# Kernel tuning notes

Hardware: AMD Instinct MI355X
Metric: run time of the kernel (lower is better)

The kernel has to match this reference:

```python
import jax, jax.numpy as jnp
import numpy as np

D_MODEL = 512
STATE_DIM = 6
D_STATE = 16
D_CONV = 4
EXPAND = 2
D_INNER = EXPAND * D_MODEL            # 1024
DT_RANK = -(-D_MODEL // 16)           # ceil(d_model/16) = 32


def setup_inputs() -> dict:
    key = jax.random.key(0)
    ks = jax.random.split(key, 12)
    s = 0.02
    return {
        "features": jax.random.normal(ks[0], (32, 2048, D_MODEL), dtype=jnp.float32),
        # Mamba params (mamba_ssm defaults: in/out_proj bias=False, conv+dt_proj bias=True)
        "in_proj_w": jax.random.normal(ks[1], (2 * D_INNER, D_MODEL), dtype=jnp.float32) * s,
        "conv_w": jax.random.normal(ks[2], (D_INNER, D_CONV), dtype=jnp.float32) * s,
        "conv_b": jnp.zeros((D_INNER,), dtype=jnp.float32),
        "x_proj_w": jax.random.normal(ks[3], (DT_RANK + 2 * D_STATE, D_INNER), dtype=jnp.float32) * s,
        "dt_proj_w": jax.random.normal(ks[4], (D_INNER, DT_RANK), dtype=jnp.float32) * s,
        "dt_proj_b": jax.random.normal(ks[5], (D_INNER,), dtype=jnp.float32) * s,
        "A_log": jnp.log(jnp.broadcast_to(jnp.arange(1, D_STATE + 1, dtype=jnp.float32), (D_INNER, D_STATE))),
        "D": jnp.ones((D_INNER,), dtype=jnp.float32),
        "out_proj_w": jax.random.normal(ks[6], (D_MODEL, D_INNER), dtype=jnp.float32) * s,
        # trailing fc head: d_model -> state_dim**2
        "fc_w": jax.random.normal(ks[7], (STATE_DIM * STATE_DIM, D_MODEL), dtype=jnp.float32) * s,
        "fc_b": jnp.zeros((STATE_DIM * STATE_DIM,), dtype=jnp.float32),
    }


def reference(features, in_proj_w, conv_w, conv_b, x_proj_w, dt_proj_w, dt_proj_b,
              A_log, D, out_proj_w, fc_w, fc_b):
    # Original loops Mamba over timesteps with seq_len=1 slices -> each timestep is
    # independent. Flatten (batch, seq) into one token axis and vectorize.
    B_, T, dm = features.shape
    f = features.reshape(B_ * T, dm)                      # (N, d_model)

    xz = f @ in_proj_w.T                                  # (N, 2*d_inner)
    x, z = jnp.split(xz, 2, axis=-1)
    # causal depthwise conv on a length-1 sequence: only the last tap contributes
    x = jax.nn.silu(x * conv_w[:, -1] + conv_b)           # (N, d_inner)

    x_dbl = x @ x_proj_w.T                                # (N, dt_rank + 2*d_state)
    dt = x_dbl[:, :DT_RANK]
    Bm = x_dbl[:, DT_RANK:DT_RANK + D_STATE]              # (N, d_state)
    Cm = x_dbl[:, DT_RANK + D_STATE:]                     # (N, d_state)
    delta = jax.nn.softplus(dt @ dt_proj_w.T + dt_proj_b) # (N, d_inner)

    # single-step selective scan with h0 = 0:
    #   h = exp(delta*A)*0 + delta*B*x ;  y = sum_s C_s h_s + D*x
    # (A_log therefore never affects the output for seq_len=1 calls)
    bc = jnp.sum(Bm * Cm, axis=-1, keepdims=True)         # (N, 1)
    y = delta * x * bc + D * x                            # (N, d_inner)
    y = y * jax.nn.silu(z)

    out = y @ out_proj_w.T                                # (N, d_model)
    A_flat = out @ fc_w.T + fc_b                          # (N, state_dim**2)
    return A_flat.reshape(B_, T, STATE_DIM, STATE_DIM)
```

## Files before the change

### kernel.cpp

```cpp
#include <hip/hip_runtime.h>

typedef unsigned short u16;
typedef unsigned int u32;
typedef __attribute__((ext_vector_type(8))) short bf16x8;
typedef __attribute__((ext_vector_type(4))) float f32x4;

#define NTOK 65536
#define DM 512
#define DI 1024

__device__ __forceinline__ float bf2f(u16 u){ u32 x=((u32)u)<<16; float f; __builtin_memcpy(&f,&x,4); return f; }
__device__ __forceinline__ u16 f2bf(float f){ u32 u; __builtin_memcpy(&u,&f,4); u += 0x7fffu + ((u>>16)&1u); return (u16)(u>>16); }
__device__ __forceinline__ float siluf(float x){ return x/(1.f+__expf(-x)); }
__device__ __forceinline__ float softplus_fast(float x){
  float l = __logf(1.f + __expf(x));
  return (x > 20.f) ? x : l;
}

__device__ __forceinline__ void gload_lds16(const void* g, void* l){
  __builtin_amdgcn_global_load_lds((const __attribute__((address_space(1))) u32*)g,
                                   (__attribute__((address_space(3))) u32*)l, 16, 0, 0);
}

__global__ void k_sentinel(float* out){ out[0] = 1.2345e6f; }

__global__ void k_cast_bf16(const float* __restrict__ in, u16* __restrict__ out, int n){
  int i = (blockIdx.x*256 + threadIdx.x)*4;
  if (i >= n) return;
  float4 v = *(const float4*)(in + i);
  ushort4 o; o.x=f2bf(v.x); o.y=f2bf(v.y); o.z=f2bf(v.z); o.w=f2bf(v.w);
  *(ushort4*)(out + i) = o;
}

__global__ void k_make_wa(const float* __restrict__ fcw, const float* __restrict__ opw,
                          u16* __restrict__ wa){
  int j = blockIdx.x*256 + threadIdx.x;
  int i = blockIdx.y;
  float s = 0.f;
  if (i < 36){
    const float* fr = fcw + i*DM;
    #pragma unroll 8
    for (int k=0;k<DM;++k) s += fr[k]*opw[(size_t)k*DI + j];
  }
  wa[(size_t)i*DI + j] = f2bf(s);
}

__global__ __launch_bounds__(512) void k_gemm_xz(
  const u16* __restrict__ A, const u16* __restrict__ B,
  const float* __restrict__ convw, const float* __restrict__ convb,
  u16* __restrict__ xp, u16* __restrict__ zs)
{
  __shared__ u16 smem[49152];
  const int tid=threadIdx.x, wv=tid>>6, ln=tid&63;
  const int l15=ln&15, l4=ln>>4, h=l15&7;
  const int d = blockIdx.x;
  const int xcd = d & 7, q = d >> 3;
  const int g = xcd + 8*(q >> 4);
  const int mcb = q & 15;
  const int r0 = g*128, c0g = mcb*128;
  const int wm=wv>>1, wn=wv&1;
  const int sr=ln>>3, scs=((ln&7)^sr)*8;
  const int chk0=(l4^h)*8, chk1=((l4+4)^h)*8;
  f32x4 acc[2][4]={};

  auto STAGE=[&](int buf, int kt){
    const int k0 = kt*64;
    u16* Ad = smem + buf*16384;
    u16* Bd = Ad + 8192;
    #pragma unroll
    for (int it=0;it<2;++it){
      int c=wv*2+it;
      gload_lds16(A + (size_t)(r0 + c*8 + sr)*DM + k0 + scs, Ad + c*512);
    }
    #pragma unroll
    for (int it=0;it<2;++it){
      int c=wv*2+it;
      gload_lds16(B + (size_t)(c0g + c*8 + sr)*DM + k0 + scs, Bd + c*512);
    }
  };

  STAGE(0,0); STAGE(1,1);
  #pragma clang loop unroll(disable)
  for (int t=0;t<8;++t){
    if (t<7) asm volatile("s_waitcnt vmcnt(4)" ::: "memory");
    else     asm volatile("s_waitcnt vmcnt(0)" ::: "memory");
    __builtin_amdgcn_s_barrier();
    __builtin_amdgcn_sched_barrier(0);
    if (t+2<8) STAGE((t+2)%3, t+2);
    const u16* Ac = smem + (t%3)*16384;
    const u16* Bc = Ac + 8192;
    #pragma unroll
    for (int kk=0;kk<2;++kk){
      const int ch = kk ? chk1 : chk0;
      bf16x8 af[2], bfr[4];
      #pragma unroll
      for (int m=0;m<2;++m) af[m]=*(const bf16x8*)(Ac + (wm*32+m*16+l15)*64 + ch);
      #pragma unroll
      for (int n=0;n<4;++n) bfr[n]=*(const bf16x8*)(Bc + (wn*64+n*16+l15)*64 + ch);
      #pragma unroll
      for (int m=0;m<2;++m)
        #pragma unroll
        for (int n=0;n<4;++n)
          acc[m][n]=__builtin_amdgcn_mfma_f32_16x16x32_bf16(af[m],bfr[n],acc[m][n],0,0,0);
    }
    __builtin_amdgcn_sched_barrier(0);
  }
  __syncthreads();

  const bool isx = (c0g < DI);
  const int cc0 = isx ? c0g : c0g - DI;
  u16* ep = smem;
  #pragma unroll
  for (int n=0;n<4;++n){
    int tcol = wn*64 + n*16 + l15;
    int gcol = c0g + tcol;
    float cw = isx ? convw[gcol*4+3] : 0.f;
    float cb = isx ? convb[gcol]     : 0.f;
    #pragma unroll
    for (int m=0;m<2;++m){
      int trow = wm*32 + m*16 + l4*4;
      #pragma unroll
      for (int r=0;r<4;++r){
        float v = acc[m][n][r];
        float o = isx ? siluf(v*cw + cb) : siluf(v);
        ep[(trow+r)*160 + tcol] = f2bf(o);
      }
    }
  }
  __syncthreads();
  const int rrow = tid>>2, qq = tid&3;
  const u16* srcp = ep + rrow*160 + qq*32;
  u16* dst = (isx ? xp : zs) + (size_t)(r0+rrow)*DI + cc0 + qq*32;
  #pragma unroll
  for (int j=0;j<4;++j)
    ((int4*)dst)[j] = ((const int4*)srcp)[j];
}

template<int EPI>
__global__ __launch_bounds__(256) void k_gemm_n64(
  const u16* __restrict__ A, const u16* __restrict__ B,
  u16* __restrict__ dtb, float* __restrict__ bc,
  const float* __restrict__ fcb, float* __restrict__ out)
{
  __shared__ u16 smem[24576];
  u16* SA = smem;
  u16* SB = smem + 16384;
  const int tid=threadIdx.x, wv=tid>>6, ln=tid&63;
  const int l15=ln&15, l4=ln>>4, h=l15&7;
  const int r0=blockIdx.x*128;
  const int wm=wv>>1, wn=wv&1;
  const int sr=ln>>3, scs=((ln&7)^sr)*8;
  const int chk0=(l4^h)*8, chk1=((l4+4)^h)*8;
  const int rA=(wm*64+l15)*64, rB=(wn*32+l15)*64;
  f32x4 acc[4][2]={};

  auto STAGE=[&](int buf, int k0){
    u16* Ad = SA + buf*8192;
    u16* Bd = SB + buf*4096;
    #pragma unroll
    for (int it=0;it<4;++it){
      int c=wv*4+it;
      gload_lds16(A + (size_t)(r0 + c*8 + sr)*DI + k0 + scs, Ad + c*512);
    }
    #pragma unroll
    for (int it=0;it<2;++it){
      int c=wv*2+it;
      gload_lds16(B + (size_t)(c*8 + sr)*DI + k0 + scs, Bd + c*512);
    }
  };

  STAGE(0, 0);
  __syncthreads();
  __builtin_amdgcn_sched_barrier(0);
  int cur = 0;
  #pragma clang loop unroll(disable)
  for (int t=0;t<16;++t){
    if (t < 15) STAGE(cur^1, (t+1)*64);
    const u16* Ac = SA + cur*8192;
    const u16* Bc = SB + cur*4096;
    #pragma unroll
    for (int kk=0;kk<2;++kk){
      const int ch = kk ? chk1 : chk0;
      bf16x8 af[4], bfr[2];
      #pragma unroll
      for (int m=0;m<4;++m) af[m]=*(const bf16x8*)(Ac + rA + m*1024 + ch);
      #pragma unroll
      for (int n=0;n<2;++n) bfr[n]=*(const bf16x8*)(Bc + rB + n*1024 + ch);
      #pragma unroll
      for (int m=0;m<4;++m)
        #pragma unroll
        for (int n=0;n<2;++n)
          acc[m][n]=__builtin_amdgcn_mfma_f32_16x16x32_bf16(af[m],bfr[n],acc[m][n],0,0,0);
    }
    __syncthreads();
    __builtin_amdgcn_sched_barrier(0);
    cur ^= 1;
  }

  if (EPI==0){
    float* W = (float*)smem;
    #pragma unroll
    for (int n=0;n<2;++n){
      int j = wn*32 + n*16 + l15;
      #pragma unroll
      for (int m=0;m<4;++m){
        int trow = wm*64 + m*16 + l4*4;
        #pragma unroll
        for (int r=0;r<4;++r)
          W[(trow+r)*68 + j] = acc[m][n][r];
      }
    }
    __syncthreads();
    const int row = tid>>1, half = tid&1;
    const float* wr = W + row*68;
    if (half==0){
      u16* dst = dtb + (size_t)(r0+row)*32;
      #pragma unroll
      for (int qv=0;qv<4;++qv){
        bf16x8 o;
        #pragma unroll
        for (int e=0;e<8;++e) o[e] = (short)f2bf(wr[qv*8+e]);
        *(bf16x8*)(dst + qv*8) = o;
      }
    } else {
      float s=0.f;
      #pragma unroll
      for (int e=0;e<16;++e) s += wr[32+e]*wr[48+e];
      bc[r0+row] = s;
    }
  } else {
    #pragma unroll
    for (int n=0;n<2;++n){
      int j = wn*32 + n*16 + l15;
      #pragma unroll
      for (int m=0;m<4;++m){
        #pragma unroll
        for (int r=0;r<4;++r){
          int t = r0 + wm*64 + m*16 + l4*4 + r;
          if (j < 36) out[(size_t)t*36 + j] = acc[m][n][r] + fcb[j];
        }
      }
    }
  }
}

__global__ __launch_bounds__(256) void k_delta_y(
  const u16* __restrict__ dtb, const u16* __restrict__ Bw,
  const float* __restrict__ dpb, const float* __restrict__ Dv,
  const float* __restrict__ bc,
  const u16* __restrict__ xp, u16* __restrict__ zy)
{
  __shared__ u16 smem[17408];
  u16* As = smem;
  u16* Bs = smem + 4096;
  const int tid=threadIdx.x, wv=tid>>6, ln=tid&63;
  const int l15=ln&15, l4=ln>>4;
  const int c0=blockIdx.x*128, r0=blockIdx.y*128;
  const int wm=wv>>1, wn=wv&1;
  const int sr=ln>>2, sc=(ln&3)*8;
  #pragma unroll
  for (int it=0;it<2;++it){
    int c=wv*2+it;
    gload_lds16(dtb + (size_t)(r0 + c*16 + sr)*32 + sc, As + c*512);
  }
  #pragma unroll
  for (int it=0;it<2;++it){
    int c=wv*2+it;
    gload_lds16(Bw + (size_t)(c0 + c*16 + sr)*32 + sc, Bs + c*512);
  }
  __syncthreads();
  __builtin_amdgcn_sched_barrier(0);
  f32x4 acc[4][4]={};
  bf16x8 af[4], bfr[4];
  #pragma unroll
  for (int m=0;m<4;++m) af[m]=*(const bf16x8*)(As + (wm*64+m*16+l15)*32 + l4*8);
  #pragma unroll
  for (int n=0;n<4;++n) bfr[n]=*(const bf16x8*)(Bs + (wn*64+n*16+l15)*32 + l4*8);
  #pragma unroll
  for (int m=0;m<4;++m)
    #pragma unroll
    for (int n=0;n<4;++n)
      acc[m][n]=__builtin_amdgcn_mfma_f32_16x16x32_bf16(af[m],bfr[n],acc[m][n],0,0,0);
  __syncthreads();
  u16* W = smem;
  #pragma unroll
  for (int n=0;n<4;++n){
    int tcol = wn*64 + n*16 + l15;
    int j = c0 + tcol;
    float dpbj = dpb[j], Dj = Dv[j];
    #pragma unroll
    for (int m=0;m<4;++m){
      int trow = wm*64 + m*16 + l4*4;
      #pragma unroll
      for (int r=0;r<4;++r){
        float delta = softplus_fast(acc[m][n][r] + dpbj);
        float w = delta*bc[r0 + trow + r] + Dj;
        W[(trow+r)*136 + tcol] = f2bf(w);
      }
    }
  }
  __syncthreads();
  const int row = tid>>1, half = tid&1;
  const u16* wp = W + row*136 + half*64;
  const size_t gbase = (size_t)(r0 + row)*DI + c0 + half*64;
  const u16* xpp = xp + gbase;
  u16* zp = zy + gbase;
  #pragma unroll
  for (int q=0;q<8;++q){
    bf16x8 wv8 = *(const bf16x8*)(wp + q*8);
    bf16x8 xv  = *(const bf16x8*)(xpp + q*8);
    bf16x8 zv  = *(const bf16x8*)(zp + q*8);
    bf16x8 ov;
    #pragma unroll
    for (int e=0;e<8;++e){
      float y = bf2f((u16)wv8[e]) * bf2f((u16)xv[e]) * bf2f((u16)zv[e]);
      ov[e] = (short)f2bf(y);
    }
    *(bf16x8*)(zp + q*8) = ov;
  }
}

extern "C" void kernel_launch(void* const* d_in, const int* in_sizes, int n_in,
                              void* d_out, int out_size, void* d_ws, size_t ws_size,
                              hipStream_t stream){
  const float* f      = (const float*)d_in[0];
  const float* inpw   = (const float*)d_in[1];
  const float* convw  = (const float*)d_in[2];
  const float* convb  = (const float*)d_in[3];
  const float* xprojw = (const float*)d_in[4];
  const float* dtpw   = (const float*)d_in[5];
  const float* dtpb   = (const float*)d_in[6];
  const float* Dv     = (const float*)d_in[8];
  const float* opw    = (const float*)d_in[9];
  const float* fcw    = (const float*)d_in[10];
  const float* fcb    = (const float*)d_in[11];
  float* out = (float*)d_out;

  char* ws = (char*)d_ws;
  size_t off = 0;
  auto alloc = [&](size_t sz)->void*{ void* p = ws + off; off += (sz + 255) & ~(size_t)255; return p; };
  u16*   fbf = (u16*)  alloc((size_t)NTOK*DM*2);
  u16*   xp  = (u16*)  alloc((size_t)NTOK*DI*2);
  u16*   zy  = (u16*)  alloc((size_t)NTOK*DI*2);
  u16*   dtb = (u16*)  alloc((size_t)NTOK*32*2);
  float* bc  = (float*)alloc((size_t)NTOK*4);
  u16*   ipw = (u16*)  alloc((size_t)2048*512*2);
  u16*   xpw = (u16*)  alloc((size_t)64*1024*2);
  u16*   dpw = (u16*)  alloc((size_t)1024*32*2);
  u16*   wa  = (u16*)  alloc((size_t)64*1024*2);
  if (off > ws_size){ k_sentinel<<<1,1,0,stream>>>(out); return; }

  k_cast_bf16<<<dim3((NTOK*DM/4)/256),256,0,stream>>>(f, fbf, NTOK*DM);
  k_cast_bf16<<<dim3((2048*512/4)/256),256,0,stream>>>(inpw, ipw, 2048*512);
  k_cast_bf16<<<dim3((64*1024/4)/256),256,0,stream>>>(xprojw, xpw, 64*1024);
  k_cast_bf16<<<dim3((1024*32/4)/256),256,0,stream>>>(dtpw, dpw, 1024*32);
  k_make_wa<<<dim3(4,64),256,0,stream>>>(fcw, opw, wa);

  k_gemm_xz<<<dim3(8192),512,0,stream>>>(fbf, ipw, convw, convb, xp, zy);
  k_gemm_n64<0><<<dim3(512),256,0,stream>>>(xp, xpw, dtb, bc, nullptr, nullptr);
  k_delta_y<<<dim3(8,512),256,0,stream>>>(dtb, dpw, dtpb, Dv, bc, xp, zy);
  k_gemm_n64<1><<<dim3(512),256,0,stream>>>(zy, wa, nullptr, nullptr, fcb, out);
}
```

Measured before the change: 583.5 us.

## Enlarge in_proj GEMM tile to 128x256 with BK=32 double buffering

The xz projection GEMM now computes a 128x256 output tile per block, 4x4 MFMA tiles per wave, instead of 128x128, which halves the block count and raises operand reuse per LDS load. The K loop moves from a 3-stage BK=64 pipeline with swizzled LDS to a 2-stage BK=32 pipeline. Shared memory is laid out k-chunk-major, so 16-byte fragment reads are contiguous. The epilogue writes through LDS in two 128-column halves. The trade-off is a shallower prefetch with a full barrier each iteration, which can expose global latency, plus higher register pressure from 64 accumulators.

```diff
diff --git a/kernel.cpp b/kernel.cpp
--- a/kernel.cpp
+++ b/kernel.cpp
@@ -50,90 +50,98 @@
   const float* __restrict__ convw, const float* __restrict__ convb,
   u16* __restrict__ xp, u16* __restrict__ zs)
 {
-  __shared__ u16 smem[49152];
+  __shared__ u16 smem[24576];
   const int tid=threadIdx.x, wv=tid>>6, ln=tid&63;
-  const int l15=ln&15, l4=ln>>4, h=l15&7;
-  const int d = blockIdx.x;
-  const int xcd = d & 7, q = d >> 3;
-  const int g = xcd + 8*(q >> 4);
-  const int mcb = q & 15;
-  const int r0 = g*128, c0g = mcb*128;
-  const int wm=wv>>1, wn=wv&1;
-  const int sr=ln>>3, scs=((ln&7)^sr)*8;
-  const int chk0=(l4^h)*8, chk1=((l4+4)^h)*8;
-  f32x4 acc[2][4]={};
+  const int l15=ln&15, l4=ln>>4;
+  const int d=blockIdx.x, xcd=d&7, q=d>>3;
+  const int g = xcd + 8*(q>>3);
+  const int cb = q & 7;
+  const int r0 = g*128, c0 = cb*256;
+  const int wm=wv>>2, wn=wv&3;
+  f32x4 acc[4][4]={};
+
+  const int arow=(wv&1)*64+ln, achk=wv>>1;
+  const int brow=(wv&3)*64+ln, bch=wv>>2;
+  const u16* Ag  = A + (size_t)(r0+arow)*DM + achk*8;
+  const u16* Bg0 = B + (size_t)(c0+brow)*DM + (bch+0)*8;
+  const u16* Bg1 = B + (size_t)(c0+brow)*DM + (bch+2)*8;
+  const int ldsA = wv*512;
+  const int ldsB0 = wv*512, ldsB1 = 4096 + wv*512;
 
   auto STAGE=[&](int buf, int kt){
-    const int k0 = kt*64;
-    u16* Ad = smem + buf*16384;
-    u16* Bd = Ad + 8192;
-    #pragma unroll
-    for (int it=0;it<2;++it){
-      int c=wv*2+it;
-      gload_lds16(A + (size_t)(r0 + c*8 + sr)*DM + k0 + scs, Ad + c*512);
-    }
-    #pragma unroll
-    for (int it=0;it<2;++it){
-      int c=wv*2+it;
-      gload_lds16(B + (size_t)(c0g + c*8 + sr)*DM + k0 + scs, Bd + c*512);
-    }
+    const int k0 = kt*32;
+    u16* Ad = smem + buf*12288;
+    u16* Bd = Ad + 4096;
+    gload_lds16(Ag  + k0, Ad + ldsA);
+    gload_lds16(Bg0 + k0, Bd + ldsB0);
+    gload_lds16(Bg1 + k0, Bd + ldsB1);
   };
 
-  STAGE(0,0); STAGE(1,1);
+  int offA[4], offB[4];
+  #pragma unroll
+  for (int m=0;m<4;++m) offA[m] = l4*1024 + (wm*64 + m*16 + l15)*8;
+  #pragma unroll
+  for (int n=0;n<4;++n) offB[n] = l4*2048 + (wn*64 + n*16 + l15)*8;
+
+  STAGE(0,0);
+  __syncthreads();
+  __builtin_amdgcn_sched_barrier(0);
   #pragma clang loop unroll(disable)
-  for (int t=0;t<8;++t){
-    if (t<7) asm volatile("s_waitcnt vmcnt(4)" ::: "memory");
-    else     asm volatile("s_waitcnt vmcnt(0)" ::: "memory");
-    __builtin_amdgcn_s_barrier();
+  for (int t=0;t<16;++t){
+    if (t<15) STAGE((t+1)&1, t+1);
+    const u16* Ac = smem + (t&1)*12288;
+    const u16* Bc = Ac + 4096;
+    bf16x8 af[4], bfr[4];
+    #pragma unroll
+    for (int m=0;m<4;++m) af[m]=*(const bf16x8*)(Ac + offA[m]);
+    #pragma unroll
+    for (int n=0;n<4;++n) bfr[n]=*(const bf16x8*)(Bc + offB[n]);
+    #pragma unroll
+    for (int m=0;m<4;++m)
+      #pragma unroll
+      for (int n=0;n<4;++n)
+        acc[m][n]=__builtin_amdgcn_mfma_f32_16x16x32_bf16(af[m],bfr[n],acc[m][n],0,0,0);
+    __syncthreads();
     __builtin_amdgcn_sched_barrier(0);
-    if (t+2<8) STAGE((t+2)%3, t+2);
-    const u16* Ac = smem + (t%3)*16384;
-    const u16* Bc = Ac + 8192;
-    #pragma unroll
-    for (int kk=0;kk<2;++kk){
-      const int ch = kk ? chk1 : chk0;
-      bf16x8 af[2], bfr[4];
-      #pragma unroll
-      for (int m=0;m<2;++m) af[m]=*(const bf16x8*)(Ac + (wm*32+m*16+l15)*64 + ch);
-      #pragma unroll
-      for (int n=0;n<4;++n) bfr[n]=*(const bf16x8*)(Bc + (wn*64+n*16+l15)*64 + ch);
-      #pragma unroll
-      for (int m=0;m<2;++m)
-        #pragma unroll
-        for (int n=0;n<4;++n)
-          acc[m][n]=__builtin_amdgcn_mfma_f32_16x16x32_bf16(af[m],bfr[n],acc[m][n],0,0,0);
-    }
-    __builtin_amdgcn_sched_barrier(0);
-  }
-  __syncthreads();
-
-  const bool isx = (c0g < DI);
-  const int cc0 = isx ? c0g : c0g - DI;
-  u16* ep = smem;
-  #pragma unroll
-  for (int n=0;n<4;++n){
-    int tcol = wn*64 + n*16 + l15;
-    int gcol = c0g + tcol;
-    float cw = isx ? convw[gcol*4+3] : 0.f;
-    float cb = isx ? convb[gcol]     : 0.f;
-    #pragma unroll
-    for (int m=0;m<2;++m){
-      int trow = wm*32 + m*16 + l4*4;
-      #pragma unroll
-      for (int r=0;r<4;++r){
-        float v = acc[m][n][r];
-        float o = isx ? siluf(v*cw + cb) : siluf(v);
-        ep[(trow+r)*160 + tcol] = f2bf(o);
-      }
-    }
-  }
-  __syncthreads();
-  const int rrow = tid>>2, qq = tid&3;
-  const u16* srcp = ep + rrow*160 + qq*32;
-  u16* dst = (isx ? xp : zs) + (size_t)(r0+rrow)*DI + cc0 + qq*32;
-  #pragma unroll
-  for (int j=0;j<4;++j)
-    ((int4*)dst)[j] = ((const int4*)srcp)[j];
+  }
+
+  const bool isx = (c0 < DI);
+  u16* W = smem;
+  #pragma unroll
+  for (int ch=0; ch<2; ++ch){
+    if ((wn>>1) == ch){
+      #pragma unroll
+      for (int n=0;n<4;++n){
+        int tcol = (wn&1)*64 + n*16 + l15;
+        int gcol = c0 + ch*128 + tcol;
+        float cw = isx ? convw[gcol*4+3] : 0.f;
+        float cbv= isx ? convb[gcol]     : 0.f;
+        #pragma unroll
+        for (int m=0;m<4;++m){
+          int trow = wm*64 + m*16 + l4*4;
+          #pragma unroll
+          for (int r=0;r<4;++r){
+            float v = acc[m][n][r];
+            float o = isx ? siluf(v*cw + cbv) : siluf(v);
+            W[(trow+r)*136 + tcol] = f2bf(o);
+          }
+        }
+      }
+    }
+    __syncthreads();
+    const int orow = tid>>2, qq = tid&3;
+    const u16* sp = W + orow*136 + qq*32;
+    const int gcol0 = c0 + ch*128 + qq*32;
+    u16* dst = (isx ? xp : zs) + (size_t)(r0+orow)*DI + (isx ? gcol0 : gcol0 - DI);
+    #pragma unroll
+    for (int j=0;j<2;++j)
+      ((int4*)dst)[j] = ((const int4*)sp)[j];
+    ((int4*)dst)[0+0] = ((const int4*)sp)[0];
+    ((int4*)dst)[1] = ((const int4*)sp)[1];
+    ((int4*)dst)[2] = ((const int4*)sp)[2];
+    ((int4*)dst)[3] = ((const int4*)sp)[3];
+    __syncthreads();
+  }
 }
 
 template<int EPI>
@@ -356,7 +364,7 @@
   k_cast_bf16<<<dim3((1024*32/4)/256),256,0,stream>>>(dtpw, dpw, 1024*32);
   k_make_wa<<<dim3(4,64),256,0,stream>>>(fcw, opw, wa);
 
-  k_gemm_xz<<<dim3(8192),512,0,stream>>>(fbf, ipw, convw, convb, xp, zy);
+  k_gemm_xz<<<dim3(4096),512,0,stream>>>(fbf, ipw, convw, convb, xp, zy);
   k_gemm_n64<0><<<dim3(512),256,0,stream>>>(xp, xpw, dtb, bc, nullptr, nullptr);
   k_delta_y<<<dim3(8,512),256,0,stream>>>(dtb, dpw, dtpb, Dv, bc, xp, zy);
   k_gemm_n64<1><<<dim3(512),256,0,stream>>>(zy, wa, nullptr, nullptr, fcb, out);
```

Measured after the change: 596.9 us. 2.3% more time.
